# Optimization experiments

Hardware: AMD Instinct MI355X
Metric: run time of the kernel (lower is better)

## Reference

```python
import jax, jax.numpy as jnp
import numpy as np

IN_F, OUT_F, USER_F = 1024, 512, 512
BSZ, S = 64, 256


def setup_inputs() -> dict:
    key = jax.random.key(0)
    k = jax.random.split(key, 7)
    X_doc = jax.random.normal(k[0], (BSZ, S, IN_F), dtype=jnp.float32)
    X_user = jax.random.normal(k[1], (BSZ, S, USER_F), dtype=jnp.float32)
    # xavier-normal-ish scaling for weights
    Wd = jax.random.normal(k[2], (OUT_F, IN_F), dtype=jnp.float32) * np.sqrt(2.0 / (IN_F + OUT_F))
    bd = jnp.zeros((OUT_F,), dtype=jnp.float32)
    Wu = jax.random.normal(k[3], (OUT_F, USER_F), dtype=jnp.float32) * np.sqrt(2.0 / (USER_F + OUT_F))
    bu = jnp.zeros((OUT_F,), dtype=jnp.float32)
    W = jax.random.normal(k[4], (OUT_F, OUT_F), dtype=jnp.float32) * np.sqrt(1.0 / OUT_F)
    return {"X_doc": X_doc, "X_user": X_user, "Wd": Wd, "bd": bd, "Wu": Wu, "bu": bu, "W": W}


def reference(X_doc, X_user, Wd, bd, Wu, bu, W):
    d = jnp.einsum('bsi,oi->bso', X_doc, Wd) + bd          # (b, s, out)
    u = jnp.einsum('bsi,oi->bso', X_user, Wu) + bu          # (b, s, out)
    d = d * jax.nn.sigmoid(u)
    u = u * jax.nn.sigmoid(d)
    att = jnp.tanh(jnp.einsum('bsd,de,bre->bsr', d, W, u))  # (b, s, s)
    score_d = jax.nn.softmax(att.mean(axis=2), axis=1)[..., None]  # (b, s, 1)
    score_u = jax.nn.softmax(att.mean(axis=1), axis=1)[..., None]  # (b, s, 1)
    attention_d = jnp.sum(score_d * d, axis=1)              # (b, out)
    attention_u = jnp.sum(score_u * u, axis=1)              # (b, out)
    return (attention_d, attention_u)
```

## Files before the change

### kernel.cpp

```cpp
#include <hip/hip_runtime.h>
#include <hip/hip_bf16.h>

#define S_ 256
#define BSZ_ 64
#define IN_F_ 1024
#define OUT_F_ 512
#define USER_F_ 512

typedef short short8 __attribute__((ext_vector_type(8)));
typedef float f32x4 __attribute__((ext_vector_type(4)));

__device__ __forceinline__ ushort f2bf(float f) {
  unsigned u = __float_as_uint(f);
  unsigned r = (u + 0x7FFFu + ((u >> 16) & 1u)) >> 16;
  return (ushort)r;
}
__device__ __forceinline__ float bf2f(unsigned hi16) {
  return __uint_as_float(hi16 << 16);
}
__device__ __forceinline__ float sigf(float x) {
  return 1.f / (1.f + __expf(-x));
}
__device__ __forceinline__ float tanh_safe(float x) {
  float ax = fabsf(x);
  float e = __expf(-2.f * ax);
  float r = (1.f - e) / (1.f + e);
  return copysignf(r, x);
}

__device__ __forceinline__ void gl_lds16(const ushort* g, ushort* l) {
  __builtin_amdgcn_global_load_lds(
      (const __attribute__((address_space(1))) void*)g,
      (__attribute__((address_space(3))) void*)l, 16, 0, 0);
}

__global__ void prep(const float* __restrict__ Xd, const float* __restrict__ Xu,
                     const float* __restrict__ Wd, const float* __restrict__ Wu,
                     const float* __restrict__ W,
                     ushort* __restrict__ Xd_bf, ushort* __restrict__ Xu_bf,
                     ushort* __restrict__ Wd_bf, ushort* __restrict__ Wu_bf,
                     ushort* __restrict__ Wt_bf, float* __restrict__ rowlog) {
  int i = blockIdx.x * 256 + threadIdx.x;
  if (i < 4194304) {
    float4 v = ((const float4*)Xd)[i];
    ushort4 o; o.x = f2bf(v.x); o.y = f2bf(v.y); o.z = f2bf(v.z); o.w = f2bf(v.w);
    ((ushort4*)Xd_bf)[i] = o;
  } else if (i < 6291456) {
    int j = i - 4194304;
    float4 v = ((const float4*)Xu)[j];
    ushort4 o; o.x = f2bf(v.x); o.y = f2bf(v.y); o.z = f2bf(v.z); o.w = f2bf(v.w);
    ((ushort4*)Xu_bf)[j] = o;
  } else if (i < 6422528) {
    int j = i - 6291456;
    float4 v = ((const float4*)Wd)[j];
    ushort4 o; o.x = f2bf(v.x); o.y = f2bf(v.y); o.z = f2bf(v.z); o.w = f2bf(v.w);
    ((ushort4*)Wd_bf)[j] = o;
  } else if (i < 6488064) {
    int j = i - 6422528;
    float4 v = ((const float4*)Wu)[j];
    ushort4 o; o.x = f2bf(v.x); o.y = f2bf(v.y); o.z = f2bf(v.z); o.w = f2bf(v.w);
    ((ushort4*)Wu_bf)[j] = o;
  } else if (i < 6750208) {
    int j = i - 6488064;
    Wt_bf[j] = f2bf(W[(j & 511) * 512 + (j >> 9)]);
  } else {
    int j = i - 6750208;
    ((float4*)rowlog)[j] = float4{0.f, 0.f, 0.f, 0.f};
  }
}

template <int ROWS>
__device__ __forceinline__ void stage_tile(const ushort* __restrict__ g, int K,
                                           ushort* lds, int w, int lane) {
  const int rin = lane >> 3;
  const int c = lane & 7;
#pragma unroll
  for (int i = 0; i < ROWS / 32; ++i) {
    int r = w * (ROWS / 4) + i * 8 + rin;
    int gc = c ^ (r & 7);
    gl_lds16(g + (long)r * K + gc * 8, lds + w * (ROWS / 4) * 64 + i * 512);
  }
}
__device__ __forceinline__ void stage_tile32(const ushort* __restrict__ g, int K,
                                             ushort* lds, int w, int lane) {
  const int rin = lane >> 3, c = lane & 7;
  int r = w * 8 + rin;
  int gc = c ^ (r & 7);
  gl_lds16(g + (long)r * K + gc * 8, lds + w * 512);
}

__device__ __forceinline__ short8 frag(const ushort* lds, int row, int kk, int q) {
  int pc = (kk * 4 + q) ^ (row & 7);
  return *(const short8*)(lds + row * 64 + pc * 8);
}
__device__ __forceinline__ short8 frag512(const ushort* lds, int row, int k,
                                          int kk, int q) {
  int pc = (kk * 4 + q) ^ (row & 7);
  return *(const short8*)(lds + row * 512 + k * 64 + pc * 8);
}

__device__ __forceinline__ void compute_step(const ushort* As, const ushort* Bs,
                                             f32x4 acc[2][4], int wr, int wc,
                                             int mlane, int q) {
#pragma unroll
  for (int kk = 0; kk < 2; ++kk) {
    short8 af[2], bfr[4];
#pragma unroll
    for (int r = 0; r < 2; ++r) af[r] = frag(As, wr * 32 + r * 16 + mlane, kk, q);
#pragma unroll
    for (int c = 0; c < 4; ++c) bfr[c] = frag(Bs, wc * 64 + c * 16 + mlane, kk, q);
#pragma unroll
    for (int r = 0; r < 2; ++r)
#pragma unroll
      for (int c = 0; c < 4; ++c)
        acc[r][c] = __builtin_amdgcn_mfma_f32_16x16x32_bf16(af[r], bfr[c], acc[r][c], 0, 0, 0);
  }
}

template <int NSTEP>
__device__ __forceinline__ void gemm_loop(const ushort* __restrict__ A,
                                          const ushort* __restrict__ B, int K,
                                          ushort* As, ushort* Bs, f32x4 acc[2][4],
                                          int w, int lane, int wr, int wc,
                                          int mlane, int q) {
#pragma unroll 1
  for (int k = 0; k < NSTEP; ++k) {
    stage_tile<64>(A + k * 64, K, As, w, lane);
    stage_tile<128>(B + k * 64, K, Bs, w, lane);
    __syncthreads();
    compute_step(As, Bs, acc, wr, wc, mlane, q);
    __syncthreads();
  }
}

#define ACC_ZERO(a)                             \
  _Pragma("unroll") for (int r = 0; r < 2; ++r) \
  _Pragma("unroll") for (int c = 0; c < 4; ++c) { \
    a[r][c][0] = 0.f; a[r][c][1] = 0.f; a[r][c][2] = 0.f; a[r][c][3] = 0.f; }

__global__ __launch_bounds__(256, 4) void gemm_du(
    const ushort* __restrict__ Xd, const ushort* __restrict__ Wd,
    const float* __restrict__ bd,
    const ushort* __restrict__ Xu, const ushort* __restrict__ Wu,
    const float* __restrict__ bu,
    ushort* __restrict__ dg, ushort* __restrict__ ug) {
  __shared__ ushort sm[12288];
  ushort* As = sm; ushort* Bs = sm + 4096;
  const int i = blockIdx.x;
  const int k8 = i & 7, j = i >> 3;
  const int by = k8 * 32 + (j >> 2), bx = j & 3;
  const int tid = threadIdx.x, lane = tid & 63, w = tid >> 6;
  const int wr = w >> 1, wc = w & 1, mlane = lane & 15, q = lane >> 4;
  const int m0 = by * 64, n0 = bx * 128;

  f32x4 accd[2][4]; ACC_ZERO(accd);
  gemm_loop<16>(Xd + (long)m0 * 1024, Wd + (long)n0 * 1024, 1024,
                As, Bs, accd, w, lane, wr, wc, mlane, q);
  f32x4 accu[2][4]; ACC_ZERO(accu);
  gemm_loop<8>(Xu + (long)m0 * 512, Wu + (long)n0 * 512, 512,
               As, Bs, accu, w, lane, wr, wc, mlane, q);

#pragma unroll
  for (int c = 0; c < 4; ++c) {
    const int gn = n0 + wc * 64 + c * 16 + mlane;
    const float bdv = bd[gn], buv = bu[gn];
#pragma unroll
    for (int r = 0; r < 2; ++r)
#pragma unroll
      for (int ii = 0; ii < 4; ++ii) {
        const int gm = m0 + wr * 32 + r * 16 + q * 4 + ii;
        const long idx = (long)gm * OUT_F_ + gn;
        float dp = accd[r][c][ii] + bdv;
        float up = accu[r][c][ii] + buv;
        float dgv = dp * sigf(up);
        float ugv = up * sigf(dgv);
        dg[idx] = f2bf(dgv);
        ug[idx] = f2bf(ugv);
      }
  }
}

__global__ __launch_bounds__(256, 2) void gemm_tatt(
    const ushort* __restrict__ dg, const ushort* __restrict__ Wt,
    const ushort* __restrict__ ug, float* __restrict__ rowlog,
    float* __restrict__ collog) {
  __shared__ ushort sm[32768];
  ushort* t_lds = sm;
  ushort* AsT = sm + 16384;
  ushort* BsT = sm + 18432;
  ushort* BsU = sm + 16384;
  const int i = blockIdx.x;
  const int xcd = i & 7, j = i >> 3;
  const int b = xcd * 8 + (j >> 3);
  const int by = j & 7;
  const int tid = threadIdx.x, lane = tid & 63, w = tid >> 6;
  const int mlane = lane & 15, q = lane >> 4;
  const ushort* dgs = dg + (long)b * (S_ * OUT_F_) + (long)by * 32 * 512;
  const ushort* ugb = ug + (long)b * (S_ * OUT_F_);

#pragma unroll 1
  for (int nc = 0; nc < 4; ++nc) {
    f32x4 acc[2][2];
#pragma unroll
    for (int r = 0; r < 2; ++r)
#pragma unroll
      for (int c = 0; c < 2; ++c) {
        acc[r][c][0] = 0.f; acc[r][c][1] = 0.f; acc[r][c][2] = 0.f; acc[r][c][3] = 0.f;
      }
    const ushort* Bw = Wt + (long)(nc * 128) * 512;
#pragma unroll 1
    for (int k = 0; k < 8; ++k) {
      stage_tile32(dgs + k * 64, 512, AsT, w, lane);
      stage_tile<128>(Bw + k * 64, 512, BsT, w, lane);
      __syncthreads();
#pragma unroll
      for (int kk = 0; kk < 2; ++kk) {
        short8 af[2], bfr[2];
#pragma unroll
        for (int r = 0; r < 2; ++r) af[r] = frag(AsT, r * 16 + mlane, kk, q);
#pragma unroll
        for (int c = 0; c < 2; ++c)
          bfr[c] = frag(BsT, w * 32 + c * 16 + mlane, kk, q);
#pragma unroll
        for (int r = 0; r < 2; ++r)
#pragma unroll
          for (int c = 0; c < 2; ++c)
            acc[r][c] = __builtin_amdgcn_mfma_f32_16x16x32_bf16(af[r], bfr[c], acc[r][c], 0, 0, 0);
      }
      __syncthreads();
    }
#pragma unroll
    for (int r = 0; r < 2; ++r)
#pragma unroll
      for (int c = 0; c < 2; ++c)
#pragma unroll
        for (int ii = 0; ii < 4; ++ii) {
          int rr = r * 16 + q * 4 + ii;
          int col = nc * 128 + w * 32 + c * 16 + mlane;
          int cc = col >> 3;
          int ph = (cc & ~7) | ((cc & 7) ^ (rr & 7));
          t_lds[rr * 512 + ph * 8 + (col & 7)] = f2bf(acc[r][c][ii]);
        }
  }

  f32x4 acc[2][4]; ACC_ZERO(acc);
#pragma unroll 1
  for (int k = 0; k < 8; ++k) {
    stage_tile<256>(ugb + k * 64, 512, BsU, w, lane);
    __syncthreads();
#pragma unroll
    for (int kk = 0; kk < 2; ++kk) {
      short8 af[2], bfr[4];
#pragma unroll
      for (int r = 0; r < 2; ++r) af[r] = frag512(t_lds, r * 16 + mlane, k, kk, q);
#pragma unroll
      for (int c = 0; c < 4; ++c)
        bfr[c] = frag(BsU, w * 64 + c * 16 + mlane, kk, q);
#pragma unroll
      for (int r = 0; r < 2; ++r)
#pragma unroll
        for (int c = 0; c < 4; ++c)
          acc[r][c] = __builtin_amdgcn_mfma_f32_16x16x32_bf16(af[r], bfr[c], acc[r][c], 0, 0, 0);
    }
    __syncthreads();
  }

  float rs[8], cs[4];
#pragma unroll
  for (int x = 0; x < 8; ++x) rs[x] = 0.f;
#pragma unroll
  for (int c = 0; c < 4; ++c) cs[c] = 0.f;
#pragma unroll
  for (int r = 0; r < 2; ++r)
#pragma unroll
    for (int c = 0; c < 4; ++c)
#pragma unroll
      for (int ii = 0; ii < 4; ++ii) {
        float v = tanh_safe(acc[r][c][ii]);
        rs[r * 4 + ii] += v;
        cs[c] += v;
      }
#pragma unroll
  for (int m = 1; m < 16; m <<= 1)
#pragma unroll
    for (int x = 0; x < 8; ++x) rs[x] += __shfl_xor(rs[x], m, 64);
#pragma unroll
  for (int m = 16; m < 64; m <<= 1)
#pragma unroll
    for (int c = 0; c < 4; ++c) cs[c] += __shfl_xor(cs[c], m, 64);

  float* rsum = (float*)BsU;
  if (tid < 32) rsum[tid] = 0.f;
  __syncthreads();
  if (mlane == 0) {
#pragma unroll
    for (int x = 0; x < 8; ++x)
      atomicAdd(&rsum[(x >> 2) * 16 + q * 4 + (x & 3)], rs[x]);
  }
  if (q == 0) {
#pragma unroll
    for (int c = 0; c < 4; ++c)
      atomicAdd(&collog[b * S_ + w * 64 + c * 16 + mlane], cs[c]);
  }
  __syncthreads();
  if (tid < 32) rowlog[b * S_ + by * 32 + tid] = rsum[tid];
}

__device__ __forceinline__ float block_max(float v, float* buf, int tid) {
  buf[tid] = v; __syncthreads();
  for (int s = 128; s > 0; s >>= 1) {
    if (tid < s) buf[tid] = fmaxf(buf[tid], buf[tid + s]);
    __syncthreads();
  }
  float r = buf[0]; __syncthreads();
  return r;
}
__device__ __forceinline__ float block_sum(float v, float* buf, int tid) {
  buf[tid] = v; __syncthreads();
  for (int s = 128; s > 0; s >>= 1) {
    if (tid < s) buf[tid] = buf[tid] + buf[tid + s];
    __syncthreads();
  }
  float r = buf[0]; __syncthreads();
  return r;
}

__global__ __launch_bounds__(256) void finalize(
    const float* __restrict__ rowlog, const float* __restrict__ collog,
    const ushort* __restrict__ dg, const ushort* __restrict__ ug,
    float* __restrict__ out) {
  __shared__ float sd[S_], su[S_], buf[S_];
  const int b = blockIdx.x >> 2, oc = blockIdx.x & 3;
  const int tid = threadIdx.x;

  const float rowmean = rowlog[b * S_ + tid] * (1.f / (float)S_);
  const float colmean = collog[b * S_ + tid] * (1.f / (float)S_);

  float md = block_max(rowmean, buf, tid);
  float ed = __expf(rowmean - md);
  float sds = block_sum(ed, buf, tid);
  sd[tid] = ed / sds;
  float mu = block_max(colmean, buf, tid);
  float eu = __expf(colmean - mu);
  float sus = block_sum(eu, buf, tid);
  su[tid] = eu / sus;
  __syncthreads();

  const int o = oc * 128 + (tid & 127);
  const ushort* src = (tid < 128) ? dg : ug;
  const float* sw = (tid < 128) ? sd : su;
  const ushort* p = src + (long)b * (S_ * OUT_F_) + o;
  float a = 0.f;
  for (int s = 0; s < S_; ++s) a += sw[s] * bf2f((unsigned)p[s * OUT_F_]);
  out[((tid < 128) ? 0 : BSZ_ * OUT_F_) + b * OUT_F_ + o] = a;
}

extern "C" void kernel_launch(void* const* d_in, const int* in_sizes, int n_in,
                              void* d_out, int out_size, void* d_ws, size_t ws_size,
                              hipStream_t stream) {
  (void)in_sizes; (void)n_in; (void)out_size; (void)ws_size;
  const float* Xd = (const float*)d_in[0];
  const float* Xu = (const float*)d_in[1];
  const float* Wd = (const float*)d_in[2];
  const float* bd = (const float*)d_in[3];
  const float* Wu = (const float*)d_in[4];
  const float* bu = (const float*)d_in[5];
  const float* W  = (const float*)d_in[6];
  float* out = (float*)d_out;
  char* ws = (char*)d_ws;

  ushort* Xd_bf  = (ushort*)(ws + 0L);
  ushort* Xu_bf  = (ushort*)(ws + 33554432L);
  ushort* Wd_bf  = (ushort*)(ws + 50331648L);
  ushort* Wu_bf  = (ushort*)(ws + 51380224L);
  ushort* Wt_bf  = (ushort*)(ws + 51904512L);
  ushort* dg     = (ushort*)(ws + 52428800L);
  ushort* ug     = (ushort*)(ws + 69206016L);
  float*  rowlog = (float*)(ws + 85983232L);
  float*  collog = (float*)(ws + 86048768L);

  prep<<<26400, 256, 0, stream>>>(Xd, Xu, Wd, Wu, W, Xd_bf, Xu_bf,
                                  Wd_bf, Wu_bf, Wt_bf, rowlog);

  dim3 blk(256);
  gemm_du<<<1024, blk, 0, stream>>>(Xd_bf, Wd_bf, bd, Xu_bf, Wu_bf, bu, dg, ug);
  gemm_tatt<<<512, blk, 0, stream>>>(dg, Wt_bf, ug, rowlog, collog);
  finalize<<<256, 256, 0, stream>>>(rowlog, collog, dg, ug, out);
}
```

Measured before the change: 222.2 us.

## Fuse fp32-to-bf16 activation conversion into GEMM A-tile loads; widen finalize loads

The GEMM now stages the fp32 activations directly into LDS and converts them to bf16 while building fragments. This removes the separate prep pass that read 96MB of fp32 and wrote a 48MB bf16 copy. In exchange the A tile in LDS doubles in size and each fragment read does extra conversion work. The finalize kernel also processes two outputs per thread with ushort2 loads over half as many blocks, which changes its memory access pattern.

```diff
diff --git a/kernel.cpp b/kernel.cpp
--- a/kernel.cpp
+++ b/kernel.cpp
@@ -18,6 +18,11 @@
 __device__ __forceinline__ float bf2f(unsigned hi16) {
   return __uint_as_float(hi16 << 16);
 }
+__device__ __forceinline__ unsigned pkbf(float a, float b) {
+  union { __hip_bfloat162 h; unsigned u; } x;
+  x.h = __float22bfloat162_rn(float2{a, b});
+  return x.u;
+}
 __device__ __forceinline__ float sigf(float x) {
   return 1.f / (1.f + __expf(-x));
 }
@@ -28,43 +33,31 @@
   return copysignf(r, x);
 }
 
-__device__ __forceinline__ void gl_lds16(const ushort* g, ushort* l) {
+__device__ __forceinline__ void gl_lds16(const void* g, void* l) {
   __builtin_amdgcn_global_load_lds(
       (const __attribute__((address_space(1))) void*)g,
       (__attribute__((address_space(3))) void*)l, 16, 0, 0);
 }
 
-__global__ void prep(const float* __restrict__ Xd, const float* __restrict__ Xu,
-                     const float* __restrict__ Wd, const float* __restrict__ Wu,
-                     const float* __restrict__ W,
-                     ushort* __restrict__ Xd_bf, ushort* __restrict__ Xu_bf,
+__global__ void prep(const float* __restrict__ Wd, const float* __restrict__ Wu,
+                     const float* __restrict__ W, float* __restrict__ rowlog,
                      ushort* __restrict__ Wd_bf, ushort* __restrict__ Wu_bf,
-                     ushort* __restrict__ Wt_bf, float* __restrict__ rowlog) {
+                     ushort* __restrict__ Wt_bf) {
   int i = blockIdx.x * 256 + threadIdx.x;
-  if (i < 4194304) {
-    float4 v = ((const float4*)Xd)[i];
+  if (i < 131072) {
+    float4 v = ((const float4*)Wd)[i];
     ushort4 o; o.x = f2bf(v.x); o.y = f2bf(v.y); o.z = f2bf(v.z); o.w = f2bf(v.w);
-    ((ushort4*)Xd_bf)[i] = o;
-  } else if (i < 6291456) {
-    int j = i - 4194304;
-    float4 v = ((const float4*)Xu)[j];
-    ushort4 o; o.x = f2bf(v.x); o.y = f2bf(v.y); o.z = f2bf(v.z); o.w = f2bf(v.w);
-    ((ushort4*)Xu_bf)[j] = o;
-  } else if (i < 6422528) {
-    int j = i - 6291456;
-    float4 v = ((const float4*)Wd)[j];
-    ushort4 o; o.x = f2bf(v.x); o.y = f2bf(v.y); o.z = f2bf(v.z); o.w = f2bf(v.w);
-    ((ushort4*)Wd_bf)[j] = o;
-  } else if (i < 6488064) {
-    int j = i - 6422528;
+    ((ushort4*)Wd_bf)[i] = o;
+  } else if (i < 196608) {
+    int j = i - 131072;
     float4 v = ((const float4*)Wu)[j];
     ushort4 o; o.x = f2bf(v.x); o.y = f2bf(v.y); o.z = f2bf(v.z); o.w = f2bf(v.w);
     ((ushort4*)Wu_bf)[j] = o;
-  } else if (i < 6750208) {
-    int j = i - 6488064;
+  } else if (i < 458752) {
+    int j = i - 196608;
     Wt_bf[j] = f2bf(W[(j & 511) * 512 + (j >> 9)]);
   } else {
-    int j = i - 6750208;
+    int j = i - 458752;
     ((float4*)rowlog)[j] = float4{0.f, 0.f, 0.f, 0.f};
   }
 }
@@ -89,6 +82,18 @@
   gl_lds16(g + (long)r * K + gc * 8, lds + w * 512);
 }
 
+__device__ __forceinline__ void stage_a32(const float* __restrict__ g, int K,
+                                          float* lds, int w, int lane) {
+  const int rl = lane >> 4;
+  const int c = lane & 15;
+#pragma unroll
+  for (int i = 0; i < 4; ++i) {
+    int r = w * 16 + i * 4 + rl;
+    int gc = (c & 8) | ((c & 7) ^ (r & 7));
+    gl_lds16(g + (long)r * K + gc * 4, lds + w * 1024 + i * 256);
+  }
+}
+
 __device__ __forceinline__ short8 frag(const ushort* lds, int row, int kk, int q) {
   int pc = (kk * 4 + q) ^ (row & 7);
   return *(const short8*)(lds + row * 64 + pc * 8);
@@ -98,6 +103,18 @@
   int pc = (kk * 4 + q) ^ (row & 7);
   return *(const short8*)(lds + row * 512 + k * 64 + pc * 8);
 }
+__device__ __forceinline__ short8 fragA32(const float* lds, int row, int kk, int q) {
+  int kc = kk * 4 + q;
+  int f0 = kc * 2, f1 = kc * 2 + 1;
+  int p0 = (f0 & 8) | ((f0 & 7) ^ (row & 7));
+  int p1 = (f1 & 8) | ((f1 & 7) ^ (row & 7));
+  const f32x4* base = (const f32x4*)(lds + row * 64);
+  f32x4 a = base[p0], b = base[p1];
+  union { short8 s; uint4 u; } o;
+  o.u.x = pkbf(a[0], a[1]); o.u.y = pkbf(a[2], a[3]);
+  o.u.z = pkbf(b[0], b[1]); o.u.w = pkbf(b[2], b[3]);
+  return o.s;
+}
 
 __device__ __forceinline__ void compute_step(const ushort* As, const ushort* Bs,
                                              f32x4 acc[2][4], int wr, int wc,
@@ -107,6 +124,23 @@
     short8 af[2], bfr[4];
 #pragma unroll
     for (int r = 0; r < 2; ++r) af[r] = frag(As, wr * 32 + r * 16 + mlane, kk, q);
+#pragma unroll
+    for (int c = 0; c < 4; ++c) bfr[c] = frag(Bs, wc * 64 + c * 16 + mlane, kk, q);
+#pragma unroll
+    for (int r = 0; r < 2; ++r)
+#pragma unroll
+      for (int c = 0; c < 4; ++c)
+        acc[r][c] = __builtin_amdgcn_mfma_f32_16x16x32_bf16(af[r], bfr[c], acc[r][c], 0, 0, 0);
+  }
+}
+__device__ __forceinline__ void compute_step_f32(const float* Asf, const ushort* Bs,
+                                                 f32x4 acc[2][4], int wr, int wc,
+                                                 int mlane, int q) {
+#pragma unroll
+  for (int kk = 0; kk < 2; ++kk) {
+    short8 af[2], bfr[4];
+#pragma unroll
+    for (int r = 0; r < 2; ++r) af[r] = fragA32(Asf, wr * 32 + r * 16 + mlane, kk, q);
 #pragma unroll
     for (int c = 0; c < 4; ++c) bfr[c] = frag(Bs, wc * 64 + c * 16 + mlane, kk, q);
 #pragma unroll
@@ -132,6 +166,21 @@
     __syncthreads();
   }
 }
+template <int NSTEP>
+__device__ __forceinline__ void gemm_loop_f32(const float* __restrict__ Af,
+                                              const ushort* __restrict__ B, int K,
+                                              float* Asf, ushort* Bs,
+                                              f32x4 acc[2][4], int w, int lane,
+                                              int wr, int wc, int mlane, int q) {
+#pragma unroll 1
+  for (int k = 0; k < NSTEP; ++k) {
+    stage_a32(Af + k * 64, K, Asf, w, lane);
+    stage_tile<128>(B + k * 64, K, Bs, w, lane);
+    __syncthreads();
+    compute_step_f32(Asf, Bs, acc, wr, wc, mlane, q);
+    __syncthreads();
+  }
+}
 
 #define ACC_ZERO(a)                             \
   _Pragma("unroll") for (int r = 0; r < 2; ++r) \
@@ -139,13 +188,14 @@
     a[r][c][0] = 0.f; a[r][c][1] = 0.f; a[r][c][2] = 0.f; a[r][c][3] = 0.f; }
 
 __global__ __launch_bounds__(256, 4) void gemm_du(
-    const ushort* __restrict__ Xd, const ushort* __restrict__ Wd,
+    const float* __restrict__ Xd, const ushort* __restrict__ Wd,
     const float* __restrict__ bd,
-    const ushort* __restrict__ Xu, const ushort* __restrict__ Wu,
+    const float* __restrict__ Xu, const ushort* __restrict__ Wu,
     const float* __restrict__ bu,
     ushort* __restrict__ dg, ushort* __restrict__ ug) {
-  __shared__ ushort sm[12288];
-  ushort* As = sm; ushort* Bs = sm + 4096;
+  __shared__ ushort sm[16384];
+  float* Asf = (float*)sm;
+  ushort* Bs = sm + 8192;
   const int i = blockIdx.x;
   const int k8 = i & 7, j = i >> 3;
   const int by = k8 * 32 + (j >> 2), bx = j & 3;
@@ -154,11 +204,11 @@
   const int m0 = by * 64, n0 = bx * 128;
 
   f32x4 accd[2][4]; ACC_ZERO(accd);
-  gemm_loop<16>(Xd + (long)m0 * 1024, Wd + (long)n0 * 1024, 1024,
-                As, Bs, accd, w, lane, wr, wc, mlane, q);
+  gemm_loop_f32<16>(Xd + (long)m0 * 1024, Wd + (long)n0 * 1024, 1024,
+                    Asf, Bs, accd, w, lane, wr, wc, mlane, q);
   f32x4 accu[2][4]; ACC_ZERO(accu);
-  gemm_loop<8>(Xu + (long)m0 * 512, Wu + (long)n0 * 512, 512,
-               As, Bs, accu, w, lane, wr, wc, mlane, q);
+  gemm_loop_f32<8>(Xu + (long)m0 * 512, Wu + (long)n0 * 512, 512,
+                   Asf, Bs, accu, w, lane, wr, wc, mlane, q);
 
 #pragma unroll
   for (int c = 0; c < 4; ++c) {
@@ -330,7 +380,7 @@
     const ushort* __restrict__ dg, const ushort* __restrict__ ug,
     float* __restrict__ out) {
   __shared__ float sd[S_], su[S_], buf[S_];
-  const int b = blockIdx.x >> 2, oc = blockIdx.x & 3;
+  const int b = blockIdx.x >> 1, half = blockIdx.x & 1;
   const int tid = threadIdx.x;
 
   const float rowmean = rowlog[b * S_ + tid] * (1.f / (float)S_);
@@ -346,13 +396,20 @@
   su[tid] = eu / sus;
   __syncthreads();
 
-  const int o = oc * 128 + (tid & 127);
-  const ushort* src = (tid < 128) ? dg : ug;
-  const float* sw = (tid < 128) ? sd : su;
+  const int arr = tid >> 7;
+  const int o = half * 256 + (tid & 127) * 2;
+  const ushort* src = arr ? ug : dg;
+  const float* sw = arr ? su : sd;
   const ushort* p = src + (long)b * (S_ * OUT_F_) + o;
-  float a = 0.f;
-  for (int s = 0; s < S_; ++s) a += sw[s] * bf2f((unsigned)p[s * OUT_F_]);
-  out[((tid < 128) ? 0 : BSZ_ * OUT_F_) + b * OUT_F_ + o] = a;
+  float a0 = 0.f, a1 = 0.f;
+#pragma unroll 4
+  for (int s = 0; s < S_; ++s) {
+    ushort2 v = *(const ushort2*)(p + (long)s * OUT_F_);
+    a0 += sw[s] * bf2f(v.x);
+    a1 += sw[s] * bf2f(v.y);
+  }
+  float* ob = out + (arr ? BSZ_ * OUT_F_ : 0) + b * OUT_F_ + o;
+  ob[0] = a0; ob[1] = a1;
 }
 
 extern "C" void kernel_launch(void* const* d_in, const int* in_sizes, int n_in,
@@ -369,21 +426,18 @@
   float* out = (float*)d_out;
   char* ws = (char*)d_ws;
 
-  ushort* Xd_bf  = (ushort*)(ws + 0L);
-  ushort* Xu_bf  = (ushort*)(ws + 33554432L);
-  ushort* Wd_bf  = (ushort*)(ws + 50331648L);
-  ushort* Wu_bf  = (ushort*)(ws + 51380224L);
-  ushort* Wt_bf  = (ushort*)(ws + 51904512L);
-  ushort* dg     = (ushort*)(ws + 52428800L);
-  ushort* ug     = (ushort*)(ws + 69206016L);
-  float*  rowlog = (float*)(ws + 85983232L);
-  float*  collog = (float*)(ws + 86048768L);
-
-  prep<<<26400, 256, 0, stream>>>(Xd, Xu, Wd, Wu, W, Xd_bf, Xu_bf,
-                                  Wd_bf, Wu_bf, Wt_bf, rowlog);
+  ushort* Wd_bf  = (ushort*)(ws + 0L);
+  ushort* Wu_bf  = (ushort*)(ws + 1048576L);
+  ushort* Wt_bf  = (ushort*)(ws + 1572864L);
+  ushort* dg     = (ushort*)(ws + 2097152L);
+  ushort* ug     = (ushort*)(ws + 18874368L);
+  float*  rowlog = (float*)(ws + 35651584L);
+  float*  collog = (float*)(ws + 35717120L);
+
+  prep<<<1824, 256, 0, stream>>>(Wd, Wu, W, rowlog, Wd_bf, Wu_bf, Wt_bf);
 
   dim3 blk(256);
-  gemm_du<<<1024, blk, 0, stream>>>(Xd_bf, Wd_bf, bd, Xu_bf, Wu_bf, bu, dg, ug);
+  gemm_du<<<1024, blk, 0, stream>>>(Xd, Wd_bf, bd, Xu, Wu_bf, bu, dg, ug);
   gemm_tatt<<<512, blk, 0, stream>>>(dg, Wt_bf, ug, rowlog, collog);
-  finalize<<<256, 256, 0, stream>>>(rowlog, collog, dg, ug, out);
-}
+  finalize<<<128, 256, 0, stream>>>(rowlog, collog, dg, ug, out);
+}
```

Result: slower. 240.2 us (+8.1%).
